# Kernel optimization log

Hardware: AMD Instinct MI355X
Metric: run time of the kernel (lower is better)

Reference implementation:

```python
import jax, jax.numpy as jnp
import numpy as np
from jax import lax

# GlobalSeed with a standard Mamba2 (SSD) core.
# C=64 feature channels, G=8 token dim, d_inner=16, d_state=16, nheads=2, headdim=8, d_conv=3.
C_FEAT, G, D_INNER, D_STATE, NHEADS, HEADDIM, D_CONV = 64, 8, 16, 16, 2, 8, 3
CONV_DIM = D_INNER + 2 * D_STATE  # 48
D_IN_PROJ = 2 * D_INNER + 2 * D_STATE + NHEADS  # 66


def setup_inputs() -> dict:
    key = jax.random.key(0)
    ks = jax.random.split(key, 16)
    B, H, W = 16, 128, 128
    s = 0.02
    return {
        "x": jax.random.normal(ks[0], (B, C_FEAT, H, W), jnp.float32),
        "tok_w": s * jax.random.normal(ks[1], (G, C_FEAT), jnp.float32),
        "tok_b": jnp.zeros((G,), jnp.float32),
        "detok_w": s * jax.random.normal(ks[2], (C_FEAT, G), jnp.float32),
        "detok_b": jnp.zeros((C_FEAT,), jnp.float32),
        "in_proj_w": s * jax.random.normal(ks[3], (D_IN_PROJ, G), jnp.float32),
        "in_proj_b": jnp.zeros((D_IN_PROJ,), jnp.float32),
        "conv_w": s * jax.random.normal(ks[4], (CONV_DIM, D_CONV), jnp.float32),
        "conv_b": jnp.zeros((CONV_DIM,), jnp.float32),
        "A_log": jnp.log(jnp.arange(1, NHEADS + 1, dtype=jnp.float32)),
        "D": jnp.ones((NHEADS,), jnp.float32),
        "dt_bias": 0.1 * jax.random.normal(ks[5], (NHEADS,), jnp.float32),
        "norm_w": jnp.ones((D_INNER,), jnp.float32),
        "out_w": s * jax.random.normal(ks[6], (G, D_INNER), jnp.float32),
        "out_b": jnp.zeros((G,), jnp.float32),
    }


def _mamba2(gt, in_proj_w, in_proj_b, conv_w, conv_b, A_log, D, dt_bias, norm_w, out_w, out_b):
    # gt: (B, L, G) tokens
    B, L, _ = gt.shape
    zxbcdt = gt @ in_proj_w.T + in_proj_b  # (B, L, 66)
    z = zxbcdt[..., :D_INNER]
    xBC = zxbcdt[..., D_INNER:D_INNER + CONV_DIM]
    dt = zxbcdt[..., D_INNER + CONV_DIM:]  # (B, L, nheads)
    # depthwise causal conv1d over L
    xBC = lax.conv_general_dilated(
        xBC.transpose(0, 2, 1), conv_w[:, None, :], (1,), [(D_CONV - 1, 0)],
        feature_group_count=CONV_DIM).transpose(0, 2, 1) + conv_b
    xBC = jax.nn.silu(xBC)
    xr = xBC[..., :D_INNER].reshape(B, L, NHEADS, HEADDIM)
    Bm = xBC[..., D_INNER:D_INNER + D_STATE]   # (B, L, N)
    Cm = xBC[..., D_INNER + D_STATE:]          # (B, L, N)
    dt = jax.nn.softplus(dt + dt_bias)          # (B, L, H)
    dec = jnp.exp(dt * (-jnp.exp(A_log)))       # (B, L, H)

    def step(h, inp):
        xt, Bt, Ct, dtt, dct = inp  # (B,H,P) (B,N) (B,N) (B,H) (B,H)
        h = dct[:, :, None, None] * h + (dtt[:, :, None] * xt)[..., None] * Bt[:, None, None, :]
        y = jnp.einsum('bhpn,bn->bhp', h, Ct)
        return h, y

    h0 = jnp.zeros((B, NHEADS, HEADDIM, D_STATE), gt.dtype)
    xs = (xr.transpose(1, 0, 2, 3), Bm.transpose(1, 0, 2), Cm.transpose(1, 0, 2),
          dt.transpose(1, 0, 2), dec.transpose(1, 0, 2))
    _, ys = lax.scan(step, h0, xs)  # (L, B, H, P)
    y = ys.transpose(1, 0, 2, 3) + D[None, None, :, None] * xr
    y = y.reshape(B, L, D_INNER)
    y = y * jax.nn.silu(z)  # gated
    y = y * lax.rsqrt(jnp.mean(y * y, axis=-1, keepdims=True) + 1e-5) * norm_w  # RMSNormGated
    return y @ out_w.T + out_b  # (B, L, G)


def reference(x, tok_w, tok_b, detok_w, detok_b, in_proj_w, in_proj_b, conv_w, conv_b,
              A_log, D, dt_bias, norm_w, out_w, out_b):
    B, C, H, W = x.shape
    L = H * W
    g = jnp.einsum('bchw,gc->bghw', x, tok_w) + tok_b[None, :, None, None]
    gt = g.reshape(B, G, L).transpose(0, 2, 1)  # (B, L, G)
    gt = _mamba2(gt, in_proj_w, in_proj_b, conv_w, conv_b, A_log, D, dt_bias, norm_w, out_w, out_b) + gt
    g2 = gt.transpose(0, 2, 1).reshape(B, G, H, W)
    return x + jnp.einsum('bghw,cg->bchw', g2, detok_w) + detok_b[None, :, None, None]
```

## Files before the change

kernel.cpp:

```cpp
#include <hip/hip_runtime.h>
#include <math.h>

#define NB 16
#define CF 64
#define LL 16384
#define GG 8
#define NH 2
#define CHN 64
#define NCH 256
#define NGRP 16

static constexpr size_t OFF_GT = 0;
static constexpr size_t OFF_U2 = OFF_GT + (size_t)NB*LL*GG;
static constexpr size_t OFF_AC = OFF_U2 + (size_t)NB*NCH*256;
static constexpr size_t OFF_PH = OFF_AC + (size_t)NB*NCH*NH;
static constexpr size_t OFF_CP = OFF_PH + (size_t)NB*NCH*256;
static constexpr size_t OFF_UG = OFF_CP + (size_t)NB*NCH*NH;
static constexpr size_t OFF_AG = OFF_UG + (size_t)NB*NGRP*256;
static constexpr size_t OFF_GH = OFF_AG + (size_t)NB*NGRP*NH;
static constexpr size_t OFF_G2 = OFF_GH + (size_t)NB*NGRP*256;
static constexpr size_t OFF_ST = OFF_G2 + (size_t)NB*LL*GG;
static constexpr size_t WS_FLOATS = OFF_ST + (size_t)NB*NCH*1792;

typedef float f32x4 __attribute__((ext_vector_type(4)));
typedef short bf16x8 __attribute__((ext_vector_type(8)));

__device__ __forceinline__ float siluf(float v){ return v / (1.f + __expf(-v)); }
__device__ __forceinline__ float softplusf(float v){ return v > 20.f ? v : log1pf(__expf(v)); }

__device__ __forceinline__ unsigned short f2bf(float f){
    unsigned int u = __float_as_uint(f);
    u += 0x7fffu + ((u >> 16) & 1u);
    return (unsigned short)(u >> 16);
}
__device__ __forceinline__ float bf2f(unsigned short s){
    return __uint_as_float(((unsigned int)s) << 16);
}
__device__ __forceinline__ unsigned int pack2bf(float lo, float hi){
    return (unsigned int)f2bf(lo) | ((unsigned int)f2bf(hi) << 16);
}
__device__ __forceinline__ unsigned int packtr(float lo, float hi){
    return (__float_as_uint(hi) & 0xffff0000u) | (__float_as_uint(lo) >> 16);
}

__device__ __forceinline__ void load8(float* d, const float* p){
    float4 a = ((const float4*)p)[0];
    float4 b = ((const float4*)p)[1];
    d[0]=a.x; d[1]=a.y; d[2]=a.z; d[3]=a.w;
    d[4]=b.x; d[5]=b.y; d[6]=b.z; d[7]=b.w;
}

__global__ __launch_bounds__(64) void k1a_tok(
    const float* __restrict__ x, const float* __restrict__ tok_w,
    const float* __restrict__ tok_b, float* __restrict__ gtw)
{
    __shared__ float s_tok[GG*CF];
    int tid = threadIdx.x;
    int b  = blockIdx.x >> 6;
    int ck = blockIdx.x & 63;
    int l0 = (ck << 8) + (tid << 2);
    for (int i = tid; i < GG*CF; i += 64) s_tok[i] = tok_w[i];
    __syncthreads();
    float acc[4][GG];
    #pragma unroll
    for (int r = 0; r < 4; ++r)
        #pragma unroll
        for (int g = 0; g < GG; ++g) acc[r][g] = tok_b[g];
    const float* xb = x + (size_t)b*CF*LL + l0;
    #pragma unroll 8
    for (int c = 0; c < CF; ++c) {
        float4 xv = *(const float4*)(xb + (size_t)c*LL);
        float xa[4] = {xv.x, xv.y, xv.z, xv.w};
        #pragma unroll
        for (int g = 0; g < GG; ++g) {
            float w = s_tok[g*CF + c];
            #pragma unroll
            for (int r = 0; r < 4; ++r) acc[r][g] = fmaf(xa[r], w, acc[r][g]);
        }
    }
    float* gp = gtw + ((size_t)b*LL + l0)*GG;
    #pragma unroll
    for (int r = 0; r < 4; ++r) {
        ((float4*)gp)[r*2+0] = make_float4(acc[r][0],acc[r][1],acc[r][2],acc[r][3]);
        ((float4*)gp)[r*2+1] = make_float4(acc[r][4],acc[r][5],acc[r][6],acc[r][7]);
    }
}

__global__ __launch_bounds__(256) void k2a_state(
    const float* __restrict__ gtw,
    const float* __restrict__ ipw, const float* __restrict__ ipb,
    const float* __restrict__ cw, const float* __restrict__ cb,
    const float* __restrict__ A_log, const float* __restrict__ dt_bias,
    float* __restrict__ stw,
    float* __restrict__ U2w, float* __restrict__ Acw)
{
    __shared__ float s_pre[48*68];
    __shared__ float s_xf[64*17], s_bf[64*17], s_cf[64*17];
    __shared__ __align__(16) unsigned short WXbf[16*72];
    __shared__ __align__(16) unsigned short BTbf[16*72];
    __shared__ float s_dt[64][2], s_nda[64][2], s_w[64][2];
    __shared__ float s_ipw[384], s_ipb2[48], s_cw2[144], s_cb2[48], s_wdt[16];

    int tid = threadIdx.x;
    int b = blockIdx.x >> 8, c = blockIdx.x & 255;
    float* stp = stw + ((size_t)(b*NCH + c))*1792;
    for (int i = tid; i < 384; i += 256) s_ipw[i] = ipw[128 + i];
    if (tid < 48) { s_ipb2[tid] = ipb[16 + tid]; s_cb2[tid] = cb[tid]; }
    else if (tid >= 64 && tid < 208) s_cw2[tid - 64] = cw[tid - 64];
    else if (tid >= 224 && tid < 240) s_wdt[tid - 224] = ipw[512 + (tid - 224)];
    __syncthreads();

    float a0e = __expf(A_log[0]), a1e = __expf(A_log[1]);
    float dtb0 = dt_bias[0], dtb1 = dt_bias[1];
    float bdt0 = ipb[64], bdt1 = ipb[65];

    int r = tid >> 2, sub = tid & 3;
    int l = c*CHN + r;
    {
        float g0[8];
        load8(g0, gtw + ((size_t)b*LL + l)*GG);
        #pragma unroll
        for (int k = 0; k < 12; ++k) {
            int ch = sub*12 + k;
            float acc = s_ipb2[ch];
            #pragma unroll
            for (int g = 0; g < 8; ++g) acc = fmaf(g0[g], s_ipw[ch*8+g], acc);
            s_pre[ch*68 + r + 2] = acc;
        }
        if (r < 2) {
            int lh = c*CHN - 1 - r, slot = 1 - r;
            if (lh >= 0) {
                float gh[8];
                load8(gh, gtw + ((size_t)b*LL + lh)*GG);
                #pragma unroll
                for (int k = 0; k < 12; ++k) {
                    int ch = sub*12 + k;
                    float acc = s_ipb2[ch];
                    #pragma unroll
                    for (int g = 0; g < 8; ++g) acc = fmaf(gh[g], s_ipw[ch*8+g], acc);
                    s_pre[ch*68 + slot] = acc;
                }
            } else {
                #pragma unroll
                for (int k = 0; k < 12; ++k) s_pre[(sub*12+k)*68 + slot] = 0.f;
            }
        }
        if (sub == 0) {
            float d0 = bdt0, d1 = bdt1;
            #pragma unroll
            for (int g = 0; g < 8; ++g) {
                d0 = fmaf(g0[g], s_wdt[g],   d0);
                d1 = fmaf(g0[g], s_wdt[8+g], d1);
            }
            float dt0 = softplusf(d0 + dtb0), dt1 = softplusf(d1 + dtb1);
            s_dt[r][0] = dt0; s_dt[r][1] = dt1;
            s_nda[r][0] = -dt0*a0e; s_nda[r][1] = -dt1*a1e;
        }
    }
    __syncthreads();

    {
        #pragma unroll
        for (int k = 0; k < 12; ++k) {
            int ch = sub*12 + k;
            float p0 = s_pre[ch*68 + r];
            float p1 = s_pre[ch*68 + r + 1];
            float p2 = s_pre[ch*68 + r + 2];
            float a = s_cb2[ch];
            a = fmaf(p0, s_cw2[ch*3+0], a);
            a = fmaf(p1, s_cw2[ch*3+1], a);
            a = fmaf(p2, s_cw2[ch*3+2], a);
            float v = siluf(a);
            if (ch < 16)      s_xf[r*17 + ch] = v;
            else if (ch < 32) s_bf[r*17 + (ch-16)] = v;
            else              s_cf[r*17 + (ch-32)] = v;
        }
    }
    if (tid < 64) {
        int rr = tid;
        float v0 = s_nda[rr][0], v1 = s_nda[rr][1];
        #pragma unroll
        for (int off = 1; off < 64; off <<= 1) {
            float t0 = __shfl_up(v0, off);
            float t1 = __shfl_up(v1, off);
            if (rr >= off) { v0 += t0; v1 += t1; }
        }
        float f0 = __shfl(v0, 63), f1 = __shfl(v1, 63);
        s_w[rr][0] = __expf(f0 - v0) * s_dt[rr][0];
        s_w[rr][1] = __expf(f1 - v1) * s_dt[rr][1];
        stp[1536 + rr*2 + 0] = v0;
        stp[1536 + rr*2 + 1] = v1;
        stp[1664 + rr*2 + 0] = s_dt[rr][0];
        stp[1664 + rr*2 + 1] = s_dt[rr][1];
        if (rr == 63)
            *(float2*)(Acw + ((size_t)b*NCH + c)*2) = make_float2(__expf(f0), __expf(f1));
    }
    __syncthreads();

    {
        unsigned int* stX = (unsigned int*)stp;
        unsigned int* stB = (unsigned int*)(stp + 512);
        unsigned int* stC = (unsigned int*)(stp + 1024);
        int half = tid >> 7;
        int t2 = tid & 127;
        int p = t2 & 15, seg = t2 >> 4;
        if (half == 0) {
            unsigned int wdW[4], wdX[4];
            #pragma unroll
            for (int j = 0; j < 4; ++j) {
                int s0 = seg*8 + 2*j, s1 = s0 + 1;
                float x0 = s_xf[s0*17 + p], x1 = s_xf[s1*17 + p];
                wdX[j] = pack2bf(x0, x1);
                wdW[j] = pack2bf(x0 * s_w[s0][p>>3], x1 * s_w[s1][p>>3]);
            }
            *(uint4*)&WXbf[p*72 + seg*8] = make_uint4(wdW[0],wdW[1],wdW[2],wdW[3]);
            *(uint4*)&stX[p*32 + seg*4]  = make_uint4(wdX[0],wdX[1],wdX[2],wdX[3]);
        } else {
            unsigned int wd[4];
            #pragma unroll
            for (int j = 0; j < 4; ++j) {
                int s0 = seg*8 + 2*j, s1 = s0 + 1;
                wd[j] = pack2bf(s_bf[s0*17 + p], s_bf[s1*17 + p]);
            }
            *(uint4*)&BTbf[p*72 + seg*8] = make_uint4(wd[0],wd[1],wd[2],wd[3]);
            int r2 = t2 >> 1, hf = t2 & 1;
            unsigned int wb[4], wc[4];
            #pragma unroll
            for (int j = 0; j < 4; ++j) {
                int c0 = hf*8 + 2*j;
                wb[j] = pack2bf(s_bf[r2*17 + c0], s_bf[r2*17 + c0 + 1]);
                wc[j] = pack2bf(s_cf[r2*17 + c0], s_cf[r2*17 + c0 + 1]);
            }
            *(uint4*)&stB[r2*8 + hf*4] = make_uint4(wb[0],wb[1],wb[2],wb[3]);
            *(uint4*)&stC[r2*8 + hf*4] = make_uint4(wc[0],wc[1],wc[2],wc[3]);
        }
    }
    __syncthreads();

    if (tid < 64) {
        int ar = tid & 15, kb = tid >> 4;
        f32x4 acc = {0.f, 0.f, 0.f, 0.f};
        #pragma unroll
        for (int kk = 0; kk < 2; ++kk) {
            bf16x8 aw = *(const bf16x8*)&WXbf[ar*72 + kk*32 + kb*8];
            bf16x8 bb = *(const bf16x8*)&BTbf[ar*72 + kk*32 + kb*8];
            acc = __builtin_amdgcn_mfma_f32_16x16x32_bf16(aw, bb, acc, 0, 0, 0);
        }
        #pragma unroll
        for (int rg = 0; rg < 4; ++rg)
            U2w[(((size_t)b*NCH + c) << 8) + (kb*4+rg)*16 + ar] = acc[rg];
    }
}

__global__ void k4c1(const float* __restrict__ U2w, const float* __restrict__ Acw,
                     float* __restrict__ phw, float* __restrict__ cpw,
                     float* __restrict__ Ugw, float* __restrict__ Agw)
{
    int b = blockIdx.x >> 4, grp = blockIdx.x & 15;
    int e = threadIdx.x, he = e >> 7;
    size_t base = (size_t)b*NCH + grp*16;
    float u[16], A[16];
    #pragma unroll
    for (int j = 0; j < 16; ++j) u[j] = U2w[((base + j) << 8) + e];
    #pragma unroll
    for (int j = 0; j < 16; ++j) A[j] = Acw[(base + j)*2 + he];
    float h = 0.f, cp = 1.f;
    #pragma unroll
    for (int j = 0; j < 16; ++j) {
        phw[((base + j) << 8) + e] = h;
        if ((e & 127) == 0) cpw[(base + j)*2 + he] = cp;
        h = fmaf(A[j], h, u[j]);
        cp *= A[j];
    }
    Ugw[(((size_t)b*NGRP + grp) << 8) + e] = h;
    if ((e & 127) == 0) Agw[((size_t)b*NGRP + grp)*2 + he] = cp;
}

__global__ void k4c2(const float* __restrict__ Ugw, const float* __restrict__ Agw,
                     float* __restrict__ ghw)
{
    int b = blockIdx.x, e = threadIdx.x, he = e >> 7;
    float u[NGRP], ag[NGRP];
    #pragma unroll
    for (int g = 0; g < NGRP; ++g) {
        u[g]  = Ugw[(((size_t)b*NGRP + g) << 8) + e];
        ag[g] = Agw[((size_t)b*NGRP + g)*2 + he];
    }
    float h = 0.f;
    #pragma unroll
    for (int g = 0; g < NGRP; ++g) {
        ghw[(((size_t)b*NGRP + g) << 8) + e] = h;
        h = fmaf(ag[g], h, u[g]);
    }
}

__global__ __launch_bounds__(256) void k2b_fused(
    const float* __restrict__ gtw,
    const float* __restrict__ ipw, const float* __restrict__ ipb,
    const float* __restrict__ Dv, const float* __restrict__ norm_w,
    const float* __restrict__ out_w, const float* __restrict__ out_b,
    const float* __restrict__ phw, const float* __restrict__ cpw,
    const float* __restrict__ ghw, const float* __restrict__ stw,
    float* __restrict__ g2w)
{
    __shared__ union {
        unsigned short Ct[64*40];
        float yb[64*20];
    } uC;
    __shared__ __align__(16) unsigned short Bt[64*40];
    __shared__ __align__(16) unsigned short XTbf[16*72];
    __shared__ __align__(16) unsigned short M2[2][64*72];
    __shared__ __align__(16) unsigned short Cp0[64*16], Cp1[64*16];
    __shared__ __align__(16) unsigned short hinT[2][8*16];
    __shared__ float s_hin[256];
    __shared__ float s_la[128];
    __shared__ float s_eti[2][64], s_etd[2][64], s_esc[2][4][4];
    __shared__ float s_zw[128], s_ow[128], s_zb[16], s_nw[16], s_ob[8];

    int tid = threadIdx.x;
    int b = blockIdx.x >> 8, c = blockIdx.x & 255;
    const float* stp = stw + ((size_t)(b*NCH + c))*1792;
    const unsigned int* stX = (const unsigned int*)stp;
    const unsigned int* stB = (const unsigned int*)(stp + 512);
    const unsigned int* stC = (const unsigned int*)(stp + 1024);

    int r = tid >> 2, sub = tid & 3;
    float g0[8];
    load8(g0, gtw + ((size_t)b*LL + c*CHN + r)*GG);
    {
        int grp = c >> 4;
        float gh  = ghw[(((size_t)b*NGRP + grp) << 8) + tid];
        float cpv = cpw[((size_t)b*NCH + c)*2 + (tid >> 7)];
        float phv = phw[(((size_t)b*NCH + c) << 8) + tid];
        s_hin[tid] = fmaf(cpv, gh, phv);
    }
    if (tid < 64) {
        int row = tid;
        *(uint4*)&uC.Ct[row*40]      = *(const uint4*)&stC[row*8];
        *(uint4*)&uC.Ct[row*40 + 8]  = *(const uint4*)&stC[row*8 + 4];
        *(uint4*)&uC.Ct[row*40 + 16] = make_uint4(0,0,0,0);
        *(uint4*)&uC.Ct[row*40 + 24] = make_uint4(0,0,0,0);
    } else if (tid < 128) {
        int row = tid - 64;
        *(uint4*)&Bt[row*40]      = *(const uint4*)&stB[row*8];
        *(uint4*)&Bt[row*40 + 8]  = *(const uint4*)&stB[row*8 + 4];
        *(uint4*)&Bt[row*40 + 16] = make_uint4(0,0,0,0);
        *(uint4*)&Bt[row*40 + 24] = make_uint4(0,0,0,0);
    } else {
        int i = tid - 128;
        int p = i >> 3, seg = i & 7;
        *(uint4*)&XTbf[p*72 + seg*8] = *(const uint4*)&stX[p*32 + seg*4];
    }
    if (tid < 128) { s_la[tid] = stp[1536 + tid]; s_zw[tid] = ipw[tid]; }
    else s_ow[tid-128] = out_w[tid-128];
    if (tid < 16) { s_zb[tid] = ipb[tid]; s_nw[tid] = norm_w[tid]; }
    else if (tid < 24) s_ob[tid-16] = out_b[tid-16];
    __syncthreads();

    float D0 = Dv[0], D1 = Dv[1];
    int lane = tid & 63, wv = tid >> 6;
    int ar = lane & 15, kb = lane >> 4;
    int trow = wv*16 + kb*4;

    f32x4 gT[4];
    {
        bf16x8 aC = *(const bf16x8*)&uC.Ct[(wv*16 + ar)*40 + kb*8];
        #pragma unroll
        for (int ss = 0; ss < 4; ++ss) {
            f32x4 g = {0.f, 0.f, 0.f, 0.f};
            if (ss <= wv) {
                bf16x8 bB = *(const bf16x8*)&Bt[(ss*16 + ar)*40 + kb*8];
                g = __builtin_amdgcn_mfma_f32_16x16x32_bf16(aC, bB, g, 0, 0, 0);
            }
            gT[ss] = g;
        }
    }
    if (tid < 128) {
        int h = tid >> 6;
        int rr = (tid & 63);
        float sc = __expf(s_la[rr*2 + h]);
        unsigned short* Cp = h ? Cp1 : Cp0;
        unsigned int* dst = (unsigned int*)&Cp[rr*16];
        #pragma unroll
        for (int j = 0; j < 8; ++j)
            dst[j] = pack2bf(sc * bf2f(uC.Ct[rr*40 + j*2]),
                             sc * bf2f(uC.Ct[rr*40 + j*2 + 1]));
        if (tid < 32) {
            int i = tid;
            int hh = i >> 4, p = (i >> 1) & 7, half = i & 1;
            unsigned int wd[4];
            #pragma unroll
            for (int j = 0; j < 4; ++j)
                wd[j] = pack2bf(s_hin[hh*128 + p*16 + half*8 + 2*j],
                                s_hin[hh*128 + p*16 + half*8 + 2*j + 1]);
            *(uint4*)&hinT[hh][p*16 + half*8] = make_uint4(wd[0],wd[1],wd[2],wd[3]);
        }
    } else {
        int i = tid - 128;
        int h = i >> 6, s = i & 63;
        int anc = s & ~15;
        float d = s_la[anc*2 + h] - s_la[s*2 + h];
        float dtv = stp[1664 + s*2 + h];
        s_eti[h][s] = __expf(-d);
        s_etd[h][s] = __expf(d) * dtv;
        if (i < 32) {
            int h2 = i >> 4, wt = (i >> 2) & 3, ws = i & 3;
            s_esc[h2][wt][ws] = (wt >= ws) ?
                __expf(s_la[(wt*16)*2 + h2] - s_la[(ws*16)*2 + h2]) : 0.f;
        }
    }
    __syncthreads();

    {
        float rowf0[4], rowf1[4];
        #pragma unroll
        for (int rg = 0; rg < 4; ++rg) {
            rowf0[rg] = s_eti[0][trow+rg];
            rowf1[rg] = s_eti[1][trow+rg];
        }
        #pragma unroll
        for (int ss = 0; ss < 4; ++ss) {
            int s = ss*16 + ar;
            if (ss > wv) {
                if (!(ar & 1)) {
                    #pragma unroll
                    for (int rg = 0; rg < 4; ++rg) {
                        *(unsigned int*)&M2[0][(trow+rg)*72 + ss*16 + ar] = 0u;
                        *(unsigned int*)&M2[1][(trow+rg)*72 + ss*16 + ar] = 0u;
                    }
                }
                continue;
            }
            float colf0 = s_esc[0][wv][ss] * s_etd[0][s];
            float colf1 = s_esc[1][wv][ss] * s_etd[1][s];
            #pragma unroll
            for (int rg = 0; rg < 4; ++rg) {
                bool keep = (s <= trow+rg);
                float m0 = keep ? rowf0[rg]*colf0*gT[ss][rg] : 0.f;
                float m1 = keep ? rowf1[rg]*colf1*gT[ss][rg] : 0.f;
                float m0p = __shfl_xor(m0, 1);
                float m1p = __shfl_xor(m1, 1);
                if (!(ar & 1)) {
                    *(unsigned int*)&M2[0][(trow+rg)*72 + ss*16 + ar] = packtr(m0, m0p);
                    *(unsigned int*)&M2[1][(trow+rg)*72 + ss*16 + ar] = packtr(m1, m1p);
                }
            }
        }
    }
    __syncthreads();

    {
        int p = ar;
        f32x4 acc0 = {0.f,0.f,0.f,0.f}, acc1 = {0.f,0.f,0.f,0.f};
        #pragma unroll
        for (int kk = 0; kk < 2; ++kk) {
            bf16x8 am0 = *(const bf16x8*)&M2[0][(wv*16 + ar)*72 + kk*32 + kb*8];
            bf16x8 am1 = *(const bf16x8*)&M2[1][(wv*16 + ar)*72 + kk*32 + kb*8];
            bf16x8 bx0 = {0,0,0,0,0,0,0,0}, bx1 = {0,0,0,0,0,0,0,0};
            if (p < 8) {
                bx0 = *(const bf16x8*)&XTbf[p*72 + kk*32 + kb*8];
                bx1 = *(const bf16x8*)&XTbf[(8+p)*72 + kk*32 + kb*8];
            }
            acc0 = __builtin_amdgcn_mfma_f32_16x16x32_bf16(am0, bx0, acc0, 0, 0, 0);
            acc1 = __builtin_amdgcn_mfma_f32_16x16x32_bf16(am1, bx1, acc1, 0, 0, 0);
        }
        bf16x8 aCp0 = {0,0,0,0,0,0,0,0}, aCp1 = {0,0,0,0,0,0,0,0};
        bf16x8 bh0 = {0,0,0,0,0,0,0,0}, bh1 = {0,0,0,0,0,0,0,0};
        if (kb < 2) {
            aCp0 = *(const bf16x8*)&Cp0[(wv*16 + ar)*16 + kb*8];
            aCp1 = *(const bf16x8*)&Cp1[(wv*16 + ar)*16 + kb*8];
            if (ar < 8) {
                bh0 = *(const bf16x8*)&hinT[0][ar*16 + kb*8];
                bh1 = *(const bf16x8*)&hinT[1][ar*16 + kb*8];
            }
        }
        acc0 = __builtin_amdgcn_mfma_f32_16x16x32_bf16(aCp0, bh0, acc0, 0, 0, 0);
        acc1 = __builtin_amdgcn_mfma_f32_16x16x32_bf16(aCp1, bh1, acc1, 0, 0, 0);
        if (p < 8) {
            #pragma unroll
            for (int rg = 0; rg < 4; ++rg) {
                int t = trow + rg;
                uC.yb[t*20 + p]     = fmaf(D0, bf2f(XTbf[p*72 + t]),     acc0[rg]);
                uC.yb[t*20 + 8 + p] = fmaf(D1, bf2f(XTbf[(8+p)*72 + t]), acc1[rg]);
            }
        }
    }
    __syncthreads();

    {
        int q = sub;
        float vv[4]; float ssq = 0.f;
        #pragma unroll
        for (int j = 0; j < 4; ++j) {
            int hp = q*4 + j;
            float zz = s_zb[hp];
            #pragma unroll
            for (int g = 0; g < 8; ++g) zz = fmaf(g0[g], s_zw[hp*8+g], zz);
            float y = uC.yb[r*20 + hp];
            float w = y * siluf(zz);
            vv[j] = w; ssq = fmaf(w, w, ssq);
        }
        ssq += __shfl_xor(ssq, 1);
        ssq += __shfl_xor(ssq, 2);
        float rn = rsqrtf(ssq*(1.f/16.f) + 1e-5f);
        float o[8];
        #pragma unroll
        for (int g = 0; g < 8; ++g) o[g] = 0.f;
        #pragma unroll
        for (int j = 0; j < 4; ++j) {
            float wj = vv[j] * rn * s_nw[q*4+j];
            #pragma unroll
            for (int g = 0; g < 8; ++g) o[g] = fmaf(wj, s_ow[g*16 + q*4 + j], o[g]);
        }
        #pragma unroll
        for (int g = 0; g < 8; ++g) {
            o[g] += __shfl_xor(o[g], 1);
            o[g] += __shfl_xor(o[g], 2);
        }
        if (q == 0) {
            #pragma unroll
            for (int g = 0; g < 8; ++g) o[g] += s_ob[g] + g0[g];
            float* gp = g2w + ((size_t)b*LL + c*CHN + r)*GG;
            ((float4*)gp)[0] = make_float4(o[0],o[1],o[2],o[3]);
            ((float4*)gp)[1] = make_float4(o[4],o[5],o[6],o[7]);
        }
    }
}

__global__ __launch_bounds__(64) void k5b_detok(
    const float* __restrict__ x, const float* __restrict__ g2w,
    const float* __restrict__ dkw, const float* __restrict__ dkb,
    float* __restrict__ outp)
{
    __shared__ float s_dw[CF*GG];
    __shared__ float s_db[CF];
    int tid = threadIdx.x;
    int b  = blockIdx.x >> 6;
    int ck = blockIdx.x & 63;
    int l0 = (ck << 8) + (tid << 2);
    for (int i = tid; i < CF*GG; i += 64) s_dw[i] = dkw[i];
    s_db[tid] = dkb[tid];
    __syncthreads();
    float g2v[4][8];
    const float* gp = g2w + ((size_t)b*LL + l0)*GG;
    #pragma unroll
    for (int r = 0; r < 4; ++r) load8(g2v[r], gp + r*GG);
    const float* xb = x + (size_t)b*CF*LL + l0;
    float* ob = outp + (size_t)b*CF*LL + l0;
    #pragma unroll 4
    for (int c = 0; c < CF; ++c) {
        float4 xv = *(const float4*)(xb + (size_t)c*LL);
        float bias = s_db[c];
        float oa[4] = {xv.x+bias, xv.y+bias, xv.z+bias, xv.w+bias};
        #pragma unroll
        for (int g = 0; g < GG; ++g) {
            float w = s_dw[c*GG+g];
            #pragma unroll
            for (int r = 0; r < 4; ++r) oa[r] = fmaf(g2v[r][g], w, oa[r]);
        }
        *(float4*)(ob + (size_t)c*LL) = make_float4(oa[0],oa[1],oa[2],oa[3]);
    }
}

extern "C" void kernel_launch(void* const* d_in, const int* in_sizes, int n_in,
                              void* d_out, int out_size, void* d_ws, size_t ws_size,
                              hipStream_t stream) {
    const float* x       = (const float*)d_in[0];
    const float* tok_w   = (const float*)d_in[1];
    const float* tok_b   = (const float*)d_in[2];
    const float* detok_w = (const float*)d_in[3];
    const float* detok_b = (const float*)d_in[4];
    const float* ipw     = (const float*)d_in[5];
    const float* ipb     = (const float*)d_in[6];
    const float* cw      = (const float*)d_in[7];
    const float* cb      = (const float*)d_in[8];
    const float* A_log   = (const float*)d_in[9];
    const float* Dv      = (const float*)d_in[10];
    const float* dt_bias = (const float*)d_in[11];
    const float* norm_w  = (const float*)d_in[12];
    const float* out_w   = (const float*)d_in[13];
    const float* out_b   = (const float*)d_in[14];
    float* ws = (float*)d_ws;
    float* outp = (float*)d_out;

    if (ws_size < WS_FLOATS * sizeof(float)) return;

    k1a_tok<<<NB*64, 64, 0, stream>>>(x, tok_w, tok_b, ws+OFF_GT);
    k2a_state<<<NB*NCH, 256, 0, stream>>>(ws+OFF_GT, ipw, ipb, cw, cb,
        A_log, dt_bias, ws+OFF_ST, ws+OFF_U2, ws+OFF_AC);
    k4c1<<<NB*NGRP, 256, 0, stream>>>(ws+OFF_U2, ws+OFF_AC,
        ws+OFF_PH, ws+OFF_CP, ws+OFF_UG, ws+OFF_AG);
    k4c2<<<NB, 256, 0, stream>>>(ws+OFF_UG, ws+OFF_AG, ws+OFF_GH);
    k2b_fused<<<NB*NCH, 256, 0, stream>>>(ws+OFF_GT, ipw, ipb,
        Dv, norm_w, out_w, out_b,
        ws+OFF_PH, ws+OFF_CP, ws+OFF_GH, ws+OFF_ST, ws+OFF_G2);
    k5b_detok<<<NB*64, 64, 0, stream>>>(x, ws+OFF_G2, detok_w, detok_b, outp);
}
```

Before: 131.6 us.

## Recompute conv-folded projections via MFMA instead of staging state through workspace

The in_proj linear and depthwise causal conv are folded into one weight matrix (in_proj rows scaled by each conv tap), so each chunk computes x/B/C (and z in the second kernel) with bf16 MFMAs over three shifted token rows. Bias terms are also folded, with a correction at the sequence start. This removes the per-chunk state buffer that k2a wrote and k2b read back (bf16 X/B/C, log-decay, dt), and k2b now recomputes these values itself. The cost is duplicated projection work in both kernels and lower precision, since bf16 inputs and weights now feed the projection.

Result: slower. 134.4 us (+2.1%).

```diff
diff --git a/kernel.cpp b/kernel.cpp
--- a/kernel.cpp
+++ b/kernel.cpp
@@ -19,8 +19,7 @@
 static constexpr size_t OFF_AG = OFF_UG + (size_t)NB*NGRP*256;
 static constexpr size_t OFF_GH = OFF_AG + (size_t)NB*NGRP*NH;
 static constexpr size_t OFF_G2 = OFF_GH + (size_t)NB*NGRP*256;
-static constexpr size_t OFF_ST = OFF_G2 + (size_t)NB*LL*GG;
-static constexpr size_t WS_FLOATS = OFF_ST + (size_t)NB*NCH*1792;
+static constexpr size_t WS_FLOATS = OFF_G2 + (size_t)NB*LL*GG;
 
 typedef float f32x4 __attribute__((ext_vector_type(4)));
 typedef short bf16x8 __attribute__((ext_vector_type(8)));
@@ -86,96 +85,111 @@
     }
 }
 
+__device__ __forceinline__ void build_W(
+    int tid, const float* ipw, const float* ipb, const float* cw, const float* cb,
+    unsigned short* Wt, float* s_bias, float* s_c0, float* s_c1, float* s_wdt)
+{
+    int col = tid & 63, kb = tid >> 6;
+    unsigned int wd0=0u, wd1=0u, wd2=0u, wd3=0u;
+    if (col < 48) {
+        if (kb < 3) {
+            float cwv = cw[col*3 + (2-kb)];
+            const float* iprow = ipw + (16+col)*8;
+            wd0 = pack2bf(iprow[0]*cwv, iprow[1]*cwv);
+            wd1 = pack2bf(iprow[2]*cwv, iprow[3]*cwv);
+            wd2 = pack2bf(iprow[4]*cwv, iprow[5]*cwv);
+            wd3 = pack2bf(iprow[6]*cwv, iprow[7]*cwv);
+        }
+    } else if (kb == 0) {
+        const float* iprow = ipw + (col-48)*8;
+        wd0 = pack2bf(iprow[0], iprow[1]);
+        wd1 = pack2bf(iprow[2], iprow[3]);
+        wd2 = pack2bf(iprow[4], iprow[5]);
+        wd3 = pack2bf(iprow[6], iprow[7]);
+    }
+    *(uint4*)&Wt[col*32 + kb*8] = make_uint4(wd0,wd1,wd2,wd3);
+    if (kb == 0) {
+        float bias;
+        if (col < 48) {
+            float w0 = cw[col*3], w1 = cw[col*3+1], w2 = cw[col*3+2];
+            float ib = ipb[16+col];
+            bias = cb[col] + ib*(w0+w1+w2);
+            s_c0[col] = ib*(w0+w1);
+            s_c1[col] = ib*w0;
+        } else bias = ipb[col-48];
+        s_bias[col] = bias;
+    } else if (kb == 1 && col < 16) s_wdt[col] = ipw[512 + col];
+}
+
 __global__ __launch_bounds__(256) void k2a_state(
     const float* __restrict__ gtw,
     const float* __restrict__ ipw, const float* __restrict__ ipb,
     const float* __restrict__ cw, const float* __restrict__ cb,
     const float* __restrict__ A_log, const float* __restrict__ dt_bias,
-    float* __restrict__ stw,
     float* __restrict__ U2w, float* __restrict__ Acw)
 {
-    __shared__ float s_pre[48*68];
-    __shared__ float s_xf[64*17], s_bf[64*17], s_cf[64*17];
-    __shared__ __align__(16) unsigned short WXbf[16*72];
+    __shared__ __align__(16) unsigned short Wt[64*32];
+    __shared__ float s_bias[64], s_c0[48], s_c1[48], s_wdt[16];
+    __shared__ __align__(16) unsigned short XTbf[16*72];
     __shared__ __align__(16) unsigned short BTbf[16*72];
     __shared__ float s_dt[64][2], s_nda[64][2], s_w[64][2];
-    __shared__ float s_ipw[384], s_ipb2[48], s_cw2[144], s_cb2[48], s_wdt[16];
 
     int tid = threadIdx.x;
     int b = blockIdx.x >> 8, c = blockIdx.x & 255;
-    float* stp = stw + ((size_t)(b*NCH + c))*1792;
-    for (int i = tid; i < 384; i += 256) s_ipw[i] = ipw[128 + i];
-    if (tid < 48) { s_ipb2[tid] = ipb[16 + tid]; s_cb2[tid] = cb[tid]; }
-    else if (tid >= 64 && tid < 208) s_cw2[tid - 64] = cw[tid - 64];
-    else if (tid >= 224 && tid < 240) s_wdt[tid - 224] = ipw[512 + (tid - 224)];
+    build_W(tid, ipw, ipb, cw, cb, Wt, s_bias, s_c0, s_c1, s_wdt);
     __syncthreads();
 
     float a0e = __expf(A_log[0]), a1e = __expf(A_log[1]);
     float dtb0 = dt_bias[0], dtb1 = dt_bias[1];
     float bdt0 = ipb[64], bdt1 = ipb[65];
 
-    int r = tid >> 2, sub = tid & 3;
-    int l = c*CHN + r;
-    {
-        float g0[8];
-        load8(g0, gtw + ((size_t)b*LL + l)*GG);
-        #pragma unroll
-        for (int k = 0; k < 12; ++k) {
-            int ch = sub*12 + k;
-            float acc = s_ipb2[ch];
-            #pragma unroll
-            for (int g = 0; g < 8; ++g) acc = fmaf(g0[g], s_ipw[ch*8+g], acc);
-            s_pre[ch*68 + r + 2] = acc;
-        }
-        if (r < 2) {
-            int lh = c*CHN - 1 - r, slot = 1 - r;
-            if (lh >= 0) {
-                float gh[8];
-                load8(gh, gtw + ((size_t)b*LL + lh)*GG);
-                #pragma unroll
-                for (int k = 0; k < 12; ++k) {
-                    int ch = sub*12 + k;
-                    float acc = s_ipb2[ch];
-                    #pragma unroll
-                    for (int g = 0; g < 8; ++g) acc = fmaf(gh[g], s_ipw[ch*8+g], acc);
-                    s_pre[ch*68 + slot] = acc;
-                }
-            } else {
-                #pragma unroll
-                for (int k = 0; k < 12; ++k) s_pre[(sub*12+k)*68 + slot] = 0.f;
-            }
-        }
-        if (sub == 0) {
-            float d0 = bdt0, d1 = bdt1;
-            #pragma unroll
-            for (int g = 0; g < 8; ++g) {
-                d0 = fmaf(g0[g], s_wdt[g],   d0);
-                d1 = fmaf(g0[g], s_wdt[8+g], d1);
-            }
-            float dt0 = softplusf(d0 + dtb0), dt1 = softplusf(d1 + dtb1);
-            s_dt[r][0] = dt0; s_dt[r][1] = dt1;
-            s_nda[r][0] = -dt0*a0e; s_nda[r][1] = -dt1*a1e;
-        }
-    }
-    __syncthreads();
-
-    {
-        #pragma unroll
-        for (int k = 0; k < 12; ++k) {
-            int ch = sub*12 + k;
-            float p0 = s_pre[ch*68 + r];
-            float p1 = s_pre[ch*68 + r + 1];
-            float p2 = s_pre[ch*68 + r + 2];
-            float a = s_cb2[ch];
-            a = fmaf(p0, s_cw2[ch*3+0], a);
-            a = fmaf(p1, s_cw2[ch*3+1], a);
-            a = fmaf(p2, s_cw2[ch*3+2], a);
-            float v = siluf(a);
-            if (ch < 16)      s_xf[r*17 + ch] = v;
-            else if (ch < 32) s_bf[r*17 + (ch-16)] = v;
-            else              s_cf[r*17 + (ch-32)] = v;
-        }
-    }
+    int lane = tid & 63, wv = tid >> 6;
+    int ar = lane & 15, kb = lane >> 4;
+    int t4 = wv*16 + kb*4;
+
+    float fr[8];
+    bf16x8 aop = {0,0,0,0,0,0,0,0};
+    int rowi = c*CHN + wv*16 + ar - kb;
+    if (kb < 3 && rowi >= 0) {
+        load8(fr, gtw + ((size_t)b*LL + rowi)*GG);
+        unsigned int* ap = (unsigned int*)&aop;
+        ap[0] = pack2bf(fr[0],fr[1]); ap[1] = pack2bf(fr[2],fr[3]);
+        ap[2] = pack2bf(fr[4],fr[5]); ap[3] = pack2bf(fr[6],fr[7]);
+    }
+    f32x4 st0, st1;
+    {
+        float bs0 = s_bias[ar], bs1 = s_bias[16+ar];
+        f32x4 c0 = {bs0,bs0,bs0,bs0};
+        f32x4 c1 = {bs1,bs1,bs1,bs1};
+        bf16x8 bw0 = *(const bf16x8*)&Wt[ar*32 + kb*8];
+        bf16x8 bw1 = *(const bf16x8*)&Wt[(16+ar)*32 + kb*8];
+        st0 = __builtin_amdgcn_mfma_f32_16x16x32_bf16(aop, bw0, c0, 0, 0, 0);
+        st1 = __builtin_amdgcn_mfma_f32_16x16x32_bf16(aop, bw1, c1, 0, 0, 0);
+    }
+    if (c == 0 && wv == 0 && kb == 0) {
+        st0[0] -= s_c0[ar];    st0[1] -= s_c1[ar];
+        st1[0] -= s_c0[16+ar]; st1[1] -= s_c1[16+ar];
+    }
+    if (kb == 0) {
+        float d0 = bdt0, d1 = bdt1;
+        #pragma unroll
+        for (int g = 0; g < 8; ++g) {
+            d0 = fmaf(fr[g], s_wdt[g],   d0);
+            d1 = fmaf(fr[g], s_wdt[8+g], d1);
+        }
+        float dt0 = softplusf(d0 + dtb0), dt1 = softplusf(d1 + dtb1);
+        int row = wv*16 + ar;
+        s_dt[row][0] = dt0; s_dt[row][1] = dt1;
+        s_nda[row][0] = -dt0*a0e; s_nda[row][1] = -dt1*a1e;
+    }
+    {
+        float v0 = siluf(st0[0]), v1 = siluf(st0[1]), v2 = siluf(st0[2]), v3 = siluf(st0[3]);
+        *(uint2*)&XTbf[ar*72 + t4] = make_uint2(pack2bf(v0,v1), pack2bf(v2,v3));
+        v0 = siluf(st1[0]); v1 = siluf(st1[1]); v2 = siluf(st1[2]); v3 = siluf(st1[3]);
+        *(uint2*)&BTbf[ar*72 + t4] = make_uint2(pack2bf(v0,v1), pack2bf(v2,v3));
+    }
+    __syncthreads();
+
     if (tid < 64) {
         int rr = tid;
         float v0 = s_nda[rr][0], v1 = s_nda[rr][1];
@@ -188,67 +202,38 @@
         float f0 = __shfl(v0, 63), f1 = __shfl(v1, 63);
         s_w[rr][0] = __expf(f0 - v0) * s_dt[rr][0];
         s_w[rr][1] = __expf(f1 - v1) * s_dt[rr][1];
-        stp[1536 + rr*2 + 0] = v0;
-        stp[1536 + rr*2 + 1] = v1;
-        stp[1664 + rr*2 + 0] = s_dt[rr][0];
-        stp[1664 + rr*2 + 1] = s_dt[rr][1];
         if (rr == 63)
             *(float2*)(Acw + ((size_t)b*NCH + c)*2) = make_float2(__expf(f0), __expf(f1));
     }
     __syncthreads();
 
-    {
-        unsigned int* stX = (unsigned int*)stp;
-        unsigned int* stB = (unsigned int*)(stp + 512);
-        unsigned int* stC = (unsigned int*)(stp + 1024);
-        int half = tid >> 7;
-        int t2 = tid & 127;
-        int p = t2 & 15, seg = t2 >> 4;
-        if (half == 0) {
-            unsigned int wdW[4], wdX[4];
-            #pragma unroll
-            for (int j = 0; j < 4; ++j) {
-                int s0 = seg*8 + 2*j, s1 = s0 + 1;
-                float x0 = s_xf[s0*17 + p], x1 = s_xf[s1*17 + p];
-                wdX[j] = pack2bf(x0, x1);
-                wdW[j] = pack2bf(x0 * s_w[s0][p>>3], x1 * s_w[s1][p>>3]);
-            }
-            *(uint4*)&WXbf[p*72 + seg*8] = make_uint4(wdW[0],wdW[1],wdW[2],wdW[3]);
-            *(uint4*)&stX[p*32 + seg*4]  = make_uint4(wdX[0],wdX[1],wdX[2],wdX[3]);
-        } else {
-            unsigned int wd[4];
-            #pragma unroll
-            for (int j = 0; j < 4; ++j) {
-                int s0 = seg*8 + 2*j, s1 = s0 + 1;
-                wd[j] = pack2bf(s_bf[s0*17 + p], s_bf[s1*17 + p]);
-            }
-            *(uint4*)&BTbf[p*72 + seg*8] = make_uint4(wd[0],wd[1],wd[2],wd[3]);
-            int r2 = t2 >> 1, hf = t2 & 1;
-            unsigned int wb[4], wc[4];
-            #pragma unroll
-            for (int j = 0; j < 4; ++j) {
-                int c0 = hf*8 + 2*j;
-                wb[j] = pack2bf(s_bf[r2*17 + c0], s_bf[r2*17 + c0 + 1]);
-                wc[j] = pack2bf(s_cf[r2*17 + c0], s_cf[r2*17 + c0 + 1]);
-            }
-            *(uint4*)&stB[r2*8 + hf*4] = make_uint4(wb[0],wb[1],wb[2],wb[3]);
-            *(uint4*)&stC[r2*8 + hf*4] = make_uint4(wc[0],wc[1],wc[2],wc[3]);
-        }
+    if (tid < 128) {
+        int p = tid >> 3, seg = tid & 7;
+        int s0 = seg*8, he = p >> 3;
+        unsigned short* xp = &XTbf[p*72 + s0];
+        unsigned int wd[4];
+        #pragma unroll
+        for (int j = 0; j < 4; ++j) {
+            float lo = bf2f(xp[2*j])   * s_w[s0+2*j][he];
+            float hi = bf2f(xp[2*j+1]) * s_w[s0+2*j+1][he];
+            wd[j] = pack2bf(lo, hi);
+        }
+        *(uint4*)xp = make_uint4(wd[0],wd[1],wd[2],wd[3]);
     }
     __syncthreads();
 
     if (tid < 64) {
-        int ar = tid & 15, kb = tid >> 4;
+        int ar2 = tid & 15, kb2 = tid >> 4;
         f32x4 acc = {0.f, 0.f, 0.f, 0.f};
         #pragma unroll
         for (int kk = 0; kk < 2; ++kk) {
-            bf16x8 aw = *(const bf16x8*)&WXbf[ar*72 + kk*32 + kb*8];
-            bf16x8 bb = *(const bf16x8*)&BTbf[ar*72 + kk*32 + kb*8];
+            bf16x8 aw = *(const bf16x8*)&XTbf[ar2*72 + kk*32 + kb2*8];
+            bf16x8 bb = *(const bf16x8*)&BTbf[ar2*72 + kk*32 + kb2*8];
             acc = __builtin_amdgcn_mfma_f32_16x16x32_bf16(aw, bb, acc, 0, 0, 0);
         }
         #pragma unroll
         for (int rg = 0; rg < 4; ++rg)
-            U2w[(((size_t)b*NCH + c) << 8) + (kb*4+rg)*16 + ar] = acc[rg];
+            U2w[(((size_t)b*NCH + c) << 8) + (kb2*4+rg)*16 + ar2] = acc[rg];
     }
 }
 
@@ -297,36 +282,31 @@
 __global__ __launch_bounds__(256) void k2b_fused(
     const float* __restrict__ gtw,
     const float* __restrict__ ipw, const float* __restrict__ ipb,
+    const float* __restrict__ cw, const float* __restrict__ cb,
+    const float* __restrict__ A_log, const float* __restrict__ dt_bias,
     const float* __restrict__ Dv, const float* __restrict__ norm_w,
     const float* __restrict__ out_w, const float* __restrict__ out_b,
     const float* __restrict__ phw, const float* __restrict__ cpw,
-    const float* __restrict__ ghw, const float* __restrict__ stw,
+    const float* __restrict__ ghw,
     float* __restrict__ g2w)
 {
-    __shared__ union {
-        unsigned short Ct[64*40];
-        float yb[64*20];
-    } uC;
+    __shared__ __align__(16) unsigned short Wt[64*32];
+    __shared__ float s_bias[64], s_c0[48], s_c1[48], s_wdt[16];
+    __shared__ union { unsigned short Ct[64*40]; float yb[64*20]; } uC;
     __shared__ __align__(16) unsigned short Bt[64*40];
     __shared__ __align__(16) unsigned short XTbf[16*72];
+    __shared__ float zf[64*17];
     __shared__ __align__(16) unsigned short M2[2][64*72];
     __shared__ __align__(16) unsigned short Cp0[64*16], Cp1[64*16];
     __shared__ __align__(16) unsigned short hinT[2][8*16];
     __shared__ float s_hin[256];
-    __shared__ float s_la[128];
+    __shared__ float s_dt[64][2], s_nda[64][2], s_la[64][2];
     __shared__ float s_eti[2][64], s_etd[2][64], s_esc[2][4][4];
-    __shared__ float s_zw[128], s_ow[128], s_zb[16], s_nw[16], s_ob[8];
+    __shared__ float s_ow[128], s_nw[16], s_ob[8];
 
     int tid = threadIdx.x;
     int b = blockIdx.x >> 8, c = blockIdx.x & 255;
-    const float* stp = stw + ((size_t)(b*NCH + c))*1792;
-    const unsigned int* stX = (const unsigned int*)stp;
-    const unsigned int* stB = (const unsigned int*)(stp + 512);
-    const unsigned int* stC = (const unsigned int*)(stp + 1024);
-
-    int r = tid >> 2, sub = tid & 3;
-    float g0[8];
-    load8(g0, gtw + ((size_t)b*LL + c*CHN + r)*GG);
+    build_W(tid, ipw, ipb, cw, cb, Wt, s_bias, s_c0, s_c1, s_wdt);
     {
         int grp = c >> 4;
         float gh  = ghw[(((size_t)b*NGRP + grp) << 8) + tid];
@@ -334,33 +314,82 @@
         float phv = phw[(((size_t)b*NCH + c) << 8) + tid];
         s_hin[tid] = fmaf(cpv, gh, phv);
     }
-    if (tid < 64) {
-        int row = tid;
-        *(uint4*)&uC.Ct[row*40]      = *(const uint4*)&stC[row*8];
-        *(uint4*)&uC.Ct[row*40 + 8]  = *(const uint4*)&stC[row*8 + 4];
-        *(uint4*)&uC.Ct[row*40 + 16] = make_uint4(0,0,0,0);
-        *(uint4*)&uC.Ct[row*40 + 24] = make_uint4(0,0,0,0);
-    } else if (tid < 128) {
-        int row = tid - 64;
-        *(uint4*)&Bt[row*40]      = *(const uint4*)&stB[row*8];
-        *(uint4*)&Bt[row*40 + 8]  = *(const uint4*)&stB[row*8 + 4];
-        *(uint4*)&Bt[row*40 + 16] = make_uint4(0,0,0,0);
-        *(uint4*)&Bt[row*40 + 24] = make_uint4(0,0,0,0);
+    if (tid < 128) {
+        *(uint4*)&Bt[(tid>>1)*40 + 16 + (tid&1)*8] = make_uint4(0,0,0,0);
+        s_ow[tid] = out_w[tid];
     } else {
-        int i = tid - 128;
-        int p = i >> 3, seg = i & 7;
-        *(uint4*)&XTbf[p*72 + seg*8] = *(const uint4*)&stX[p*32 + seg*4];
-    }
-    if (tid < 128) { s_la[tid] = stp[1536 + tid]; s_zw[tid] = ipw[tid]; }
-    else s_ow[tid-128] = out_w[tid-128];
-    if (tid < 16) { s_zb[tid] = ipb[tid]; s_nw[tid] = norm_w[tid]; }
-    else if (tid < 24) s_ob[tid-16] = out_b[tid-16];
-    __syncthreads();
-
+        int t2 = tid - 128;
+        *(uint4*)&uC.Ct[(t2>>1)*40 + 16 + (t2&1)*8] = make_uint4(0,0,0,0);
+        if (t2 < 16) s_nw[t2] = norm_w[t2];
+        else if (t2 < 24) s_ob[t2-16] = out_b[t2-16];
+    }
+    __syncthreads();
+
+    float a0e = __expf(A_log[0]), a1e = __expf(A_log[1]);
+    float dtb0 = dt_bias[0], dtb1 = dt_bias[1];
+    float bdt0 = ipb[64], bdt1 = ipb[65];
     float D0 = Dv[0], D1 = Dv[1];
+
     int lane = tid & 63, wv = tid >> 6;
     int ar = lane & 15, kb = lane >> 4;
     int trow = wv*16 + kb*4;
+
+    float fr[8];
+    bf16x8 aop = {0,0,0,0,0,0,0,0};
+    int rowi = c*CHN + wv*16 + ar - kb;
+    if (kb < 3 && rowi >= 0) {
+        load8(fr, gtw + ((size_t)b*LL + rowi)*GG);
+        unsigned int* ap = (unsigned int*)&aop;
+        ap[0] = pack2bf(fr[0],fr[1]); ap[1] = pack2bf(fr[2],fr[3]);
+        ap[2] = pack2bf(fr[4],fr[5]); ap[3] = pack2bf(fr[6],fr[7]);
+    }
+    f32x4 st0, st1, st2, st3;
+    {
+        float b0 = s_bias[ar], b1 = s_bias[16+ar], b2 = s_bias[32+ar], b3 = s_bias[48+ar];
+        f32x4 c0v = {b0,b0,b0,b0}, c1v = {b1,b1,b1,b1};
+        f32x4 c2v = {b2,b2,b2,b2}, c3v = {b3,b3,b3,b3};
+        st0 = __builtin_amdgcn_mfma_f32_16x16x32_bf16(aop, *(const bf16x8*)&Wt[ar*32 + kb*8],       c0v, 0,0,0);
+        st1 = __builtin_amdgcn_mfma_f32_16x16x32_bf16(aop, *(const bf16x8*)&Wt[(16+ar)*32 + kb*8],  c1v, 0,0,0);
+        st2 = __builtin_amdgcn_mfma_f32_16x16x32_bf16(aop, *(const bf16x8*)&Wt[(32+ar)*32 + kb*8],  c2v, 0,0,0);
+        st3 = __builtin_amdgcn_mfma_f32_16x16x32_bf16(aop, *(const bf16x8*)&Wt[(48+ar)*32 + kb*8],  c3v, 0,0,0);
+    }
+    if (c == 0 && wv == 0 && kb == 0) {
+        st0[0] -= s_c0[ar];    st0[1] -= s_c1[ar];
+        st1[0] -= s_c0[16+ar]; st1[1] -= s_c1[16+ar];
+        st2[0] -= s_c0[32+ar]; st2[1] -= s_c1[32+ar];
+    }
+    if (kb == 0) {
+        float d0 = bdt0, d1 = bdt1;
+        #pragma unroll
+        for (int g = 0; g < 8; ++g) {
+            d0 = fmaf(fr[g], s_wdt[g],   d0);
+            d1 = fmaf(fr[g], s_wdt[8+g], d1);
+        }
+        float dt0 = softplusf(d0 + dtb0), dt1 = softplusf(d1 + dtb1);
+        int row = wv*16 + ar;
+        s_dt[row][0] = dt0; s_dt[row][1] = dt1;
+        s_nda[row][0] = -dt0*a0e; s_nda[row][1] = -dt1*a1e;
+    }
+    {
+        float v0 = siluf(st0[0]), v1 = siluf(st0[1]), v2 = siluf(st0[2]), v3 = siluf(st0[3]);
+        *(uint2*)&XTbf[ar*72 + trow] = make_uint2(pack2bf(v0,v1), pack2bf(v2,v3));
+        #pragma unroll
+        for (int rg = 0; rg < 4; ++rg) {
+            float vB = siluf(st1[rg]);
+            float vC = siluf(st2[rg]);
+            float pB = __shfl_xor(vB, 1);
+            float pC = __shfl_xor(vC, 1);
+            if (!(ar & 1)) {
+                *(unsigned int*)&Bt[(trow+rg)*40 + ar]    = pack2bf(vB, pB);
+                *(unsigned int*)&uC.Ct[(trow+rg)*40 + ar] = pack2bf(vC, pC);
+            }
+            zf[(trow+rg)*17 + ar] = st3[rg];
+        }
+    }
+    float g0[8];
+    if ((tid & 3) == 0)
+        load8(g0, gtw + ((size_t)b*LL + c*CHN + (tid>>2))*GG);
+    __syncthreads();
 
     f32x4 gT[4];
     {
@@ -375,10 +404,23 @@
             gT[ss] = g;
         }
     }
+    if (tid < 64) {
+        int rr = tid;
+        float v0 = s_nda[rr][0], v1 = s_nda[rr][1];
+        #pragma unroll
+        for (int off = 1; off < 64; off <<= 1) {
+            float t0 = __shfl_up(v0, off);
+            float t1 = __shfl_up(v1, off);
+            if (rr >= off) { v0 += t0; v1 += t1; }
+        }
+        s_la[rr][0] = v0; s_la[rr][1] = v1;
+    }
+    __syncthreads();
+
     if (tid < 128) {
         int h = tid >> 6;
-        int rr = (tid & 63);
-        float sc = __expf(s_la[rr*2 + h]);
+        int rr = tid & 63;
+        float sc = __expf(s_la[rr][h]);
         unsigned short* Cp = h ? Cp1 : Cp0;
         unsigned int* dst = (unsigned int*)&Cp[rr*16];
         #pragma unroll
@@ -399,14 +441,13 @@
         int i = tid - 128;
         int h = i >> 6, s = i & 63;
         int anc = s & ~15;
-        float d = s_la[anc*2 + h] - s_la[s*2 + h];
-        float dtv = stp[1664 + s*2 + h];
+        float d = s_la[anc][h] - s_la[s][h];
         s_eti[h][s] = __expf(-d);
-        s_etd[h][s] = __expf(d) * dtv;
+        s_etd[h][s] = __expf(d) * s_dt[s][h];
         if (i < 32) {
             int h2 = i >> 4, wt = (i >> 2) & 3, ws = i & 3;
             s_esc[h2][wt][ws] = (wt >= ws) ?
-                __expf(s_la[(wt*16)*2 + h2] - s_la[(ws*16)*2 + h2]) : 0.f;
+                __expf(s_la[wt*16][h2] - s_la[ws*16][h2]) : 0.f;
         }
     }
     __syncthreads();
@@ -488,14 +529,12 @@
     __syncthreads();
 
     {
-        int q = sub;
+        int r = tid >> 2, q = tid & 3;
         float vv[4]; float ssq = 0.f;
         #pragma unroll
         for (int j = 0; j < 4; ++j) {
             int hp = q*4 + j;
-            float zz = s_zb[hp];
-            #pragma unroll
-            for (int g = 0; g < 8; ++g) zz = fmaf(g0[g], s_zw[hp*8+g], zz);
+            float zz = zf[r*17 + hp];
             float y = uC.yb[r*20 + hp];
             float w = y * siluf(zz);
             vv[j] = w; ssq = fmaf(w, w, ssq);
@@ -587,12 +626,12 @@
 
     k1a_tok<<<NB*64, 64, 0, stream>>>(x, tok_w, tok_b, ws+OFF_GT);
     k2a_state<<<NB*NCH, 256, 0, stream>>>(ws+OFF_GT, ipw, ipb, cw, cb,
-        A_log, dt_bias, ws+OFF_ST, ws+OFF_U2, ws+OFF_AC);
+        A_log, dt_bias, ws+OFF_U2, ws+OFF_AC);
     k4c1<<<NB*NGRP, 256, 0, stream>>>(ws+OFF_U2, ws+OFF_AC,
         ws+OFF_PH, ws+OFF_CP, ws+OFF_UG, ws+OFF_AG);
     k4c2<<<NB, 256, 0, stream>>>(ws+OFF_UG, ws+OFF_AG, ws+OFF_GH);
-    k2b_fused<<<NB*NCH, 256, 0, stream>>>(ws+OFF_GT, ipw, ipb,
-        Dv, norm_w, out_w, out_b,
-        ws+OFF_PH, ws+OFF_CP, ws+OFF_GH, ws+OFF_ST, ws+OFF_G2);
+    k2b_fused<<<NB*NCH, 256, 0, stream>>>(ws+OFF_GT, ipw, ipb, cw, cb,
+        A_log, dt_bias, Dv, norm_w, out_w, out_b,
+        ws+OFF_PH, ws+OFF_CP, ws+OFF_GH, ws+OFF_G2);
     k5b_detok<<<NB*64, 64, 0, stream>>>(x, ws+OFF_G2, detok_w, detok_b, outp);
 }
```
